# Optimization experiments

Measured on AMD Instinct MI355X. Metric: run time of the kernel, lower is better.

## Reference

```python
import jax, jax.numpy as jnp
import numpy as np

IN_F, OUT_F, GROUP, KROT, PACK, BATCH = 4096, 14336, 128, 8, 8, 16


def _pack_nibbles(nib):
    # nib: int32 in [0,16) with shape [R, C]; pack 8 consecutive cols into one int32
    shifts = 4 * jnp.arange(PACK, dtype=jnp.int32)
    return jnp.sum(nib.reshape(nib.shape[0], -1, PACK) << shifts, axis=-1).astype(jnp.int32)


def setup_inputs() -> dict:
    key = jax.random.key(0)
    ks = jax.random.split(key, 7)
    n_groups = IN_F // GROUP
    x = jax.random.normal(ks[0], (BATCH, IN_F), dtype=jnp.float16)
    theta = (0.1 * jax.random.normal(ks[1], (KROT, IN_F // 2), dtype=jnp.float32)).astype(jnp.float16)
    # each rotation round pairs channels via a permutation: (pairs[k,2i], pairs[k,2i+1])
    pairs = jnp.stack([
        jax.random.permutation(jax.random.fold_in(ks[2], k), IN_F)
        for k in range(KROT)
    ]).astype(jnp.int32)
    channel_scales = (1.0 + 0.01 * jax.random.normal(ks[3], (1, IN_F), dtype=jnp.float32)).astype(jnp.float16)
    qweight = _pack_nibbles(jax.random.randint(ks[4], (IN_F, OUT_F), 0, 16, dtype=jnp.int32))
    qzeros = _pack_nibbles(jax.random.randint(ks[5], (n_groups, OUT_F), 0, 16, dtype=jnp.int32))
    scales = (0.001 + 0.01 * jax.random.uniform(ks[6], (n_groups, OUT_F), dtype=jnp.float32)).astype(jnp.float16)
    return {"x": x, "theta": theta, "pairs": pairs, "channel_scales": channel_scales,
            "qweight": qweight, "qzeros": qzeros, "scales": scales}


def _rotate(x, theta, pairs, channel_scales):
    # KROT rounds of pairwise Givens rotations, then per-channel scaling
    cos = jnp.cos(theta.astype(jnp.float32)).astype(x.dtype)  # [KROT, IN/2]
    sin = jnp.sin(theta.astype(jnp.float32)).astype(x.dtype)
    for k in range(theta.shape[0]):
        ia, ib = pairs[k, 0::2], pairs[k, 1::2]
        a, b = x[..., ia], x[..., ib]
        x = x.at[..., ia].set(cos[k] * a - sin[k] * b).at[..., ib].set(sin[k] * a + cos[k] * b)
    return x * channel_scales


def _dequant(qweight, qzeros, scales, group_size, dtype):
    shifts = 4 * jnp.arange(PACK, dtype=jnp.int32)
    iw = ((qweight[:, :, None] >> shifts) & 0xF).reshape(qweight.shape[0], -1)  # [IN, OUT]
    iz = ((qzeros[:, :, None] >> shifts) & 0xF).reshape(qzeros.shape[0], -1)    # [n_groups, OUT]
    w = (iw - jnp.repeat(iz, group_size, axis=0)).astype(dtype)
    return w * jnp.repeat(scales, group_size, axis=0)


def reference(x, theta, pairs, channel_scales, qweight, qzeros, scales):
    group_size = x.shape[-1] // qzeros.shape[0]
    xr = _rotate(x, theta, pairs, channel_scales)
    w = _dequant(qweight, qzeros, scales, group_size, xr.dtype)  # [IN, OUT] fp16
    return xr @ w  # [BATCH, OUT]
```

## Files before the change

### kernel.cpp

```cpp
#include <hip/hip_runtime.h>
#include <cstdint>

#define IN_F   4096
#define OUT_F  14336
#define GROUP  128
#define KROT   8
#define BATCH  16
#define NJP    1792
#define NG     32

typedef __attribute__((ext_vector_type(8))) short short8;
typedef __attribute__((ext_vector_type(4))) float f32x4;

__device__ uint32_t g_xa[BATCH * IN_F / 2];
__device__ float    g_part[4 * BATCH * OUT_F];

static __device__ __forceinline__ unsigned short f2bf(float f) {
    union { float f; uint32_t i; } v; v.f = f;
    uint32_t u = v.i;
    uint32_t r = u + 0x7FFFu + ((u >> 16) & 1u);
    return (unsigned short)(r >> 16);
}

__global__ __launch_bounds__(1024) void k_rotate(
    const float* __restrict__ x,
    const float* __restrict__ theta,
    const int*   __restrict__ pairs,
    const float* __restrict__ cscale)
{
    __shared__ float row[IN_F];
    const int b   = blockIdx.x;
    const int tid = threadIdx.x;

    int2  ij0[KROT], ij1[KROT];
    float c0[KROT], s0[KROT], c1[KROT], s1[KROT];
#pragma unroll
    for (int k = 0; k < KROT; ++k) {
        const int2*  pk = (const int2*)(pairs + k * IN_F);
        const float* tk = theta + k * (IN_F / 2);
        ij0[k] = pk[tid];
        ij1[k] = pk[tid + 1024];
        __sincosf(tk[tid],        &s0[k], &c0[k]);
        __sincosf(tk[tid + 1024], &s1[k], &c1[k]);
    }

    for (int i = tid; i < IN_F; i += 1024) row[i] = x[b * IN_F + i];
    __syncthreads();

#pragma unroll
    for (int k = 0; k < KROT; ++k) {
        float a0 = row[ij0[k].x], b0 = row[ij0[k].y];
        float a1 = row[ij1[k].x], b1 = row[ij1[k].y];
        row[ij0[k].x] = c0[k] * a0 - s0[k] * b0;
        row[ij0[k].y] = s0[k] * a0 + c0[k] * b0;
        row[ij1[k].x] = c1[k] * a1 - s1[k] * b1;
        row[ij1[k].y] = s1[k] * a1 + c1[k] * b1;
        __syncthreads();
    }

    for (int i = tid; i < IN_F / 2; i += 1024) {
        float v0 = row[2 * i]     * cscale[2 * i];
        float v1 = row[2 * i + 1] * cscale[2 * i + 1];
        g_xa[b * (IN_F / 2) + i] =
            (uint32_t)f2bf(v0) | ((uint32_t)f2bf(v1) << 16);
    }
}

__global__ __launch_bounds__(256) void k_gemm(
    const int*   __restrict__ qweight,
    const int*   __restrict__ qzeros,
    const float* __restrict__ scales)
{
    __shared__ uint4 ldsb[128 * 17];

    const int tid   = threadIdx.x;
    const int bn    = blockIdx.x % 112;
    const int bk    = blockIdx.x / 112;
    const int n0    = bn * 128;
    const int jp0   = n0 >> 3;
    const int jp    = tid & 15;
    const int koct  = tid >> 4;
    const int lane  = tid & 63;
    const int wv    = tid >> 6;
    const int mrow  = lane & 15;
    const int quad  = lane >> 4;
    const int xsw   = koct ^ (jp & 7);

    f32x4 m0 = {0.f, 0.f, 0.f, 0.f};
    f32x4 m1 = {0.f, 0.f, 0.f, 0.f};

    const int nl0 = wv * 32 + mrow;
    const int nl1 = nl0 + 16;
    const int sw0 = (nl0 >> 3) & 7;
    const int sw1 = (nl1 >> 3) & 7;

    for (int st = 0; st < 8; ++st) {
        const int g   = bk * 8 + st;
        const int kr0 = g * GROUP + koct * 8;

        uint32_t wvv[8];
#pragma unroll
        for (int i = 0; i < 8; ++i)
            wvv[i] = (uint32_t)qweight[(size_t)(kr0 + i) * NJP + jp0 + jp];
        const uint32_t zw = (uint32_t)qzeros[(size_t)g * NJP + jp0 + jp];

#pragma unroll
        for (int c = 0; c < 8; ++c) {
            const int iz = (int)((zw >> (4 * c)) & 15u);
            uint4 cell;
            uint32_t pk[4];
#pragma unroll
            for (int h = 0; h < 4; ++h) {
                union { float f; uint32_t u; } a, b;
                a.f = (float)((int)((wvv[2 * h]     >> (4 * c)) & 15u) - iz);
                b.f = (float)((int)((wvv[2 * h + 1] >> (4 * c)) & 15u) - iz);
                pk[h] = (a.u >> 16) | (b.u & 0xFFFF0000u);
            }
            cell.x = pk[0]; cell.y = pk[1]; cell.z = pk[2]; cell.w = pk[3];
            ldsb[(jp * 8 + c) * 17 + xsw] = cell;
        }
        __syncthreads();

        f32x4 ga = {0.f, 0.f, 0.f, 0.f};
        f32x4 gb = {0.f, 0.f, 0.f, 0.f};
        const uint32_t* ap = g_xa + mrow * (IN_F / 2)
                           + ((bk * 1024 + st * 128 + quad * 8) >> 1);
#pragma unroll
        for (int kt = 0; kt < 4; ++kt) {
            union { uint4 q; short8 s; } af, b0, b1;
            af.q = *(const uint4*)(ap + kt * 16);
            const int ko = kt * 4 + quad;
            b0.q = ldsb[nl0 * 17 + (ko ^ sw0)];
            b1.q = ldsb[nl1 * 17 + (ko ^ sw1)];
            ga = __builtin_amdgcn_mfma_f32_16x16x32_bf16(af.s, b0.s, ga, 0, 0, 0);
            gb = __builtin_amdgcn_mfma_f32_16x16x32_bf16(af.s, b1.s, gb, 0, 0, 0);
        }
        const float s0 = scales[(size_t)g * OUT_F + n0 + nl0];
        const float s1 = scales[(size_t)g * OUT_F + n0 + nl1];
        m0 += s0 * ga;
        m1 += s1 * gb;
        __syncthreads();
    }

    float* pp = g_part + (size_t)bk * BATCH * OUT_F;
#pragma unroll
    for (int r = 0; r < 4; ++r) {
        const int row = quad * 4 + r;
        pp[(size_t)row * OUT_F + n0 + nl0] = m0[r];
        pp[(size_t)row * OUT_F + n0 + nl1] = m1[r];
    }
}

__global__ __launch_bounds__(128) void k_reduce(float* __restrict__ out)
{
    const int t = blockIdx.x * 128 + threadIdx.x;
    const size_t j = (size_t)t * 4;
    float4 a = *(const float4*)(g_part + j);
    float4 b = *(const float4*)(g_part + (size_t)BATCH * OUT_F + j);
    float4 c = *(const float4*)(g_part + (size_t)2 * BATCH * OUT_F + j);
    float4 d = *(const float4*)(g_part + (size_t)3 * BATCH * OUT_F + j);
    float4 s;
    s.x = (a.x + b.x) + (c.x + d.x);
    s.y = (a.y + b.y) + (c.y + d.y);
    s.z = (a.z + b.z) + (c.z + d.z);
    s.w = (a.w + b.w) + (c.w + d.w);
    *(float4*)(out + j) = s;
}

extern "C" void kernel_launch(void* const* d_in, const int* in_sizes, int n_in,
                              void* d_out, int out_size, void* d_ws, size_t ws_size,
                              hipStream_t stream) {
    const float* x       = (const float*)d_in[0];
    const float* theta   = (const float*)d_in[1];
    const int*   pairs   = (const int*)d_in[2];
    const float* cscale  = (const float*)d_in[3];
    const int*   qweight = (const int*)d_in[4];
    const int*   qzeros  = (const int*)d_in[5];
    const float* scales  = (const float*)d_in[6];
    float*       out     = (float*)d_out;
    (void)d_ws; (void)ws_size;

    k_rotate<<<16, 1024, 0, stream>>>(x, theta, pairs, cscale);
    k_gemm<<<448, 256, 0, stream>>>(qweight, qzeros, scales);
    k_reduce<<<(BATCH * OUT_F) / (128 * 4), 128, 0, stream>>>(out);
}
```

Measured before the change: 110.2 us.

## Fold zero-point subtraction into per-group row sums with magic-number bf16 dequant

Weights are now dequantized by OR-ing the nibble into the bf16 pattern 0x4300, which gives 128+q directly and drops the int-to-float conversion per element. The zero point and the 128 bias are removed afterwards using per-group row sums of the activations, computed in the rotate kernel with wave shuffles and stored in a new global buffer. Scales, zeros and row sums for all eight groups are loaded before the loop, and activation fragments are loaded before the LDS barrier. The cost is more registers and some precision loss, because a large offset term is subtracted from the accumulated product.

After: 107.6 us. 1.03x faster.

```diff
diff --git a/kernel.cpp b/kernel.cpp
--- a/kernel.cpp
+++ b/kernel.cpp
@@ -13,6 +13,7 @@
 typedef __attribute__((ext_vector_type(4))) float f32x4;
 
 __device__ uint32_t g_xa[BATCH * IN_F / 2];
+__device__ float    g_rs[NG * BATCH];
 __device__ float    g_part[4 * BATCH * OUT_F];
 
 static __device__ __forceinline__ unsigned short f2bf(float f) {
@@ -20,6 +21,9 @@
     uint32_t u = v.i;
     uint32_t r = u + 0x7FFFu + ((u >> 16) & 1u);
     return (unsigned short)(r >> 16);
+}
+static __device__ __forceinline__ float bf2f(uint32_t u16) {
+    union { uint32_t i; float f; } v; v.i = u16 << 16; return v.f;
 }
 
 __global__ __launch_bounds__(1024) void k_rotate(
@@ -58,11 +62,28 @@
         __syncthreads();
     }
 
-    for (int i = tid; i < IN_F / 2; i += 1024) {
-        float v0 = row[2 * i]     * cscale[2 * i];
-        float v1 = row[2 * i + 1] * cscale[2 * i + 1];
-        g_xa[b * (IN_F / 2) + i] =
-            (uint32_t)f2bf(v0) | ((uint32_t)f2bf(v1) << 16);
+    float p0, p1;
+    {
+        int i = tid;
+        uint32_t lo = f2bf(row[2 * i]     * cscale[2 * i]);
+        uint32_t hi = f2bf(row[2 * i + 1] * cscale[2 * i + 1]);
+        g_xa[b * (IN_F / 2) + i] = lo | (hi << 16);
+        p0 = bf2f(lo) + bf2f(hi);
+        i = tid + 1024;
+        lo = f2bf(row[2 * i]     * cscale[2 * i]);
+        hi = f2bf(row[2 * i + 1] * cscale[2 * i + 1]);
+        g_xa[b * (IN_F / 2) + i] = lo | (hi << 16);
+        p1 = bf2f(lo) + bf2f(hi);
+    }
+#pragma unroll
+    for (int m = 1; m < 64; m <<= 1) {
+        p0 += __shfl_xor(p0, m, 64);
+        p1 += __shfl_xor(p1, m, 64);
+    }
+    if ((tid & 63) == 0) {
+        const int w = tid >> 6;
+        g_rs[w * BATCH + b]        = p0;
+        g_rs[(16 + w) * BATCH + b] = p1;
     }
 }
 
@@ -86,35 +107,54 @@
     const int quad  = lane >> 4;
     const int xsw   = koct ^ (jp & 7);
 
-    f32x4 m0 = {0.f, 0.f, 0.f, 0.f};
-    f32x4 m1 = {0.f, 0.f, 0.f, 0.f};
-
     const int nl0 = wv * 32 + mrow;
     const int nl1 = nl0 + 16;
     const int sw0 = (nl0 >> 3) & 7;
     const int sw1 = (nl1 >> 3) & 7;
 
+    float s0v[8], s1v[8], zf0[8], zf1[8];
+    f32x4 rsv[8];
+    {
+        const int jz0 = jp0 + (nl0 >> 3);
+        const int jz1 = jp0 + (nl1 >> 3);
+        const int sh  = 4 * (mrow & 7);
+#pragma unroll
+        for (int g = 0; g < 8; ++g) {
+            const int gg = bk * 8 + g;
+            s0v[g] = scales[(size_t)gg * OUT_F + n0 + nl0];
+            s1v[g] = scales[(size_t)gg * OUT_F + n0 + nl1];
+            zf0[g] = 128.0f + (float)(((uint32_t)qzeros[gg * NJP + jz0] >> sh) & 15u);
+            zf1[g] = 128.0f + (float)(((uint32_t)qzeros[gg * NJP + jz1] >> sh) & 15u);
+            rsv[g] = *(const f32x4*)(g_rs + gg * BATCH + quad * 4);
+        }
+    }
+
+    f32x4 m0 = {0.f, 0.f, 0.f, 0.f};
+    f32x4 m1 = {0.f, 0.f, 0.f, 0.f};
+
     for (int st = 0; st < 8; ++st) {
         const int g   = bk * 8 + st;
         const int kr0 = g * GROUP + koct * 8;
 
-        uint32_t wvv[8];
+        uint32_t wc[8];
 #pragma unroll
         for (int i = 0; i < 8; ++i)
-            wvv[i] = (uint32_t)qweight[(size_t)(kr0 + i) * NJP + jp0 + jp];
-        const uint32_t zw = (uint32_t)qzeros[(size_t)g * NJP + jp0 + jp];
+            wc[i] = (uint32_t)qweight[(size_t)(kr0 + i) * NJP + jp0 + jp];
+
+        uint4 ac[4];
+        const uint32_t* apst = g_xa + mrow * (IN_F / 2) + bk * 512 + st * 64 + quad * 4;
+#pragma unroll
+        for (int kt = 0; kt < 4; ++kt) ac[kt] = *(const uint4*)(apst + kt * 16);
 
 #pragma unroll
         for (int c = 0; c < 8; ++c) {
-            const int iz = (int)((zw >> (4 * c)) & 15u);
             uint4 cell;
             uint32_t pk[4];
 #pragma unroll
             for (int h = 0; h < 4; ++h) {
-                union { float f; uint32_t u; } a, b;
-                a.f = (float)((int)((wvv[2 * h]     >> (4 * c)) & 15u) - iz);
-                b.f = (float)((int)((wvv[2 * h + 1] >> (4 * c)) & 15u) - iz);
-                pk[h] = (a.u >> 16) | (b.u & 0xFFFF0000u);
+                uint32_t lo = (wc[2 * h]     >> (4 * c)) & 15u;
+                uint32_t hi = (wc[2 * h + 1] >> (4 * c)) & 15u;
+                pk[h] = 0x43004300u | lo | (hi << 16);
             }
             cell.x = pk[0]; cell.y = pk[1]; cell.z = pk[2]; cell.w = pk[3];
             ldsb[(jp * 8 + c) * 17 + xsw] = cell;
@@ -123,22 +163,24 @@
 
         f32x4 ga = {0.f, 0.f, 0.f, 0.f};
         f32x4 gb = {0.f, 0.f, 0.f, 0.f};
-        const uint32_t* ap = g_xa + mrow * (IN_F / 2)
-                           + ((bk * 1024 + st * 128 + quad * 8) >> 1);
 #pragma unroll
         for (int kt = 0; kt < 4; ++kt) {
             union { uint4 q; short8 s; } af, b0, b1;
-            af.q = *(const uint4*)(ap + kt * 16);
+            af.q = ac[kt];
             const int ko = kt * 4 + quad;
             b0.q = ldsb[nl0 * 17 + (ko ^ sw0)];
             b1.q = ldsb[nl1 * 17 + (ko ^ sw1)];
             ga = __builtin_amdgcn_mfma_f32_16x16x32_bf16(af.s, b0.s, ga, 0, 0, 0);
             gb = __builtin_amdgcn_mfma_f32_16x16x32_bf16(af.s, b1.s, gb, 0, 0, 0);
         }
-        const float s0 = scales[(size_t)g * OUT_F + n0 + nl0];
-        const float s1 = scales[(size_t)g * OUT_F + n0 + nl1];
-        m0 += s0 * ga;
-        m1 += s1 * gb;
+
+        const float t0 = s0v[st] * zf0[st];
+        const float t1 = s1v[st] * zf1[st];
+#pragma unroll
+        for (int r = 0; r < 4; ++r) {
+            m0[r] = fmaf(s0v[st], ga[r], fmaf(-t0, rsv[st][r], m0[r]));
+            m1[r] = fmaf(s1v[st], gb[r], fmaf(-t1, rsv[st][r], m1[r]));
+        }
         __syncthreads();
     }
 
```
